# Optimization experiments

Hardware: AMD Instinct MI355X
Metric: run time of the kernel (lower is better)

The kernel has to match this reference:

```python
import jax, jax.numpy as jnp
import numpy as np

A_DIM = 12      # action dim (half of augmented state)
N_STEPS = 10    # Heun ODE steps (Flow.N)
P = 0.95        # mixing coefficient in _Heun_method


def _mlp(x, obs, t, W1, b1, W2, b2, W3, b3, W4, b4):
    h = jnp.concatenate([x, obs, t], axis=-1)
    h = jnp.tanh(h @ W1 + b1)
    h = jnp.tanh(h @ W2 + b2)
    h = jnp.tanh(h @ W3 + b3)
    return h @ W4 + b4


def _heun(obs, x, params):
    # Flow._Heun_method: sequential Heun integration of the augmented state.
    z = x[..., :A_DIM]
    y = x[..., A_DIM:]
    dt = 1.0 / N_STEPS
    tshape = x.shape[:-1] + (1,)

    def step(carry, i):
        z, y = carry
        t = jnp.ones(tshape, x.dtype) * (i / N_STEPS)
        z_t = _mlp(y, obs, t, *params)
        z_in = z + z_t * dt
        y_t = _mlp(z_in, obs, t, *params)
        y_in = y + y_t * dt
        z_new = P * z_in + (1.0 - P) * y_in
        y_new = P * y_in + (1.0 - P) * z_new
        return (z_new, y_new), None

    (z, y), _ = jax.lax.scan(step, (z, y), jnp.arange(N_STEPS, dtype=x.dtype))
    return jnp.concatenate([z, y], axis=-1)


def setup_inputs() -> dict:
    key = jax.random.key(0)
    ks = jax.random.split(key, 8)
    B, OBS, H, A = 2048, 48, 256, A_DIM
    din = A + OBS + 1  # 61
    s = 0.05  # small init scale to keep tanh unsaturated
    return {
        "observations": jax.random.normal(ks[0], (B, OBS), jnp.float32),
        "action_aug_0": jax.random.normal(ks[1], (B, 2 * A), jnp.float32),
        "W1": s * jax.random.normal(ks[2], (din, H), jnp.float32),
        "b1": jnp.zeros((H,), jnp.float32),
        "W2": s * jax.random.normal(ks[3], (H, H), jnp.float32),
        "b2": jnp.zeros((H,), jnp.float32),
        "W3": s * jax.random.normal(ks[4], (H, H), jnp.float32),
        "b3": jnp.zeros((H,), jnp.float32),
        "W4": s * jax.random.normal(ks[5], (H, A), jnp.float32),
        "b4": jnp.zeros((A,), jnp.float32),
        "jac": 1,
    }


def reference(observations, action_aug_0, W1, b1, W2, b2, W3, b3, W4, b4, jac):
    params = (W1, b1, W2, b2, W3, b3, W4, b4)
    action_aug = _heun(observations, action_aug_0, params)
    d = action_aug_0.shape[-1]
    # Normal(0, I) log prob summed over dims
    log_probs = -0.5 * jnp.sum(action_aug_0 ** 2, axis=-1) - 0.5 * d * jnp.log(2.0 * jnp.pi)
    if jac:
        single = lambda o, x: _heun(o, x, params)  # per-sample (obs_dim,), (2a,)
        J = jax.vmap(jax.jacrev(single, argnums=1))(observations, action_aug_0)  # (B, 2a, 2a)
        _, logabsdet = jnp.linalg.slogdet(J)  # = log|det J|
        log_probs = log_probs - logabsdet
    return action_aug, log_probs
```

## Files before the change

kernel.cpp:

```cpp
#include <hip/hip_runtime.h>
#include <hip/hip_bf16.h>


typedef unsigned short ushort_t;
typedef float f32x4 __attribute__((ext_vector_type(4)));
typedef short s16x8 __attribute__((ext_vector_type(8)));

#define NB      2048
#define OBS_D   48
#define XDIM    24
#define NSTEPS  10
#define DT      0.1f
#define PP      0.95f

#define W1U 0
#define W2U 16384
#define W3U 81920
#define W4U 147456
#define FRAG_BLOCKS 592
#define LP_BLOCKS 8

#define LDS_BUFA 0
#define LDS_BUFB 8192
#define LDS_AIN  16384
#define LDS_PART 18432
#define LDS_TOTAL 27648

__device__ __forceinline__ ushort_t f2bf(float f) {
  unsigned u = __builtin_bit_cast(unsigned, f);
  u += 0x7fffu + ((u >> 16) & 1u);
  return (ushort_t)(u >> 16);
}

__device__ __forceinline__ float tanh_fast(float x) {
  float e = __builtin_amdgcn_exp2f(x * 2.885390081777927f);
  return 1.f - 2.f * __builtin_amdgcn_rcpf(1.f + e);
}

__device__ __forceinline__ int ain_byte(int r, int c) {
  int cb = ((c >> 5) << 6) | ((c & 15) << 2) | (((c >> 4) & 1) << 1);
  return r * 128 + (cb ^ ((r & 7) << 4));
}

__global__ void prep_kernel(const float* __restrict__ W1, const float* __restrict__ b1,
                            const float* __restrict__ W2, const float* __restrict__ W3,
                            const float* __restrict__ W4, const float* __restrict__ x0,
                            const int* __restrict__ jac, float* __restrict__ out,
                            ushort_t* __restrict__ ws) {
  int bid = blockIdx.x;
  int tid = threadIdx.x;
  if (bid < FRAG_BLOCKS) {
    int e = bid * 256 + tid;
    float val = 0.f;
    if (e < 16384) {
      int kt = e >> 13; int r = e & 8191;
      int nt = r >> 9, l = (r >> 3) & 63, j = r & 7;
      int k = kt * 32 + ((l >> 4) << 2) + (j >> 1) + ((j & 1) << 4);
      int col = nt * 16 + (l & 15);
      val = (k < 61) ? W1[k * 256 + col] : ((k == 61) ? b1[col] : 0.f);
    } else if (e < 81920) {
      int e2 = e - 16384;
      int kt = e2 >> 13; int r = e2 & 8191;
      int nt = r >> 9, l = (r >> 3) & 63, j = r & 7;
      int k = kt * 32 + ((l >> 4) << 2) + (j >> 1) + ((j & 1) << 4);
      int col = nt * 16 + (l & 15);
      val = W2[k * 256 + col];
    } else if (e < 147456) {
      int e2 = e - 81920;
      int kt = e2 >> 13; int r = e2 & 8191;
      int nt = r >> 9, l = (r >> 3) & 63, j = r & 7;
      int k = kt * 32 + ((l >> 4) << 2) + (j >> 1) + ((j & 1) << 4);
      int col = nt * 16 + (l & 15);
      val = W3[k * 256 + col];
    } else {
      int e2 = e - 147456;
      int kt = e2 >> 9; int r = e2 & 511;
      int l = (r >> 3) & 63, j = r & 7;
      int k = kt * 32 + ((l >> 4) << 2) + (j >> 1) + ((j & 1) << 4);
      int col = l & 15;
      val = (col < 12) ? W4[k * 12 + col] : 0.f;
    }
    ws[e] = f2bf(val);
  } else {
    int s = (bid - FRAG_BLOCKS) * 256 + tid;
    float acc = 0.f;
    #pragma unroll 4
    for (int j = 0; j < XDIM; ++j) { float v = x0[s * XDIM + j]; acc += v * v; }
    float C = (jac[0] != 0) ? -9.744134143900015f : -22.054524796912143f;
    out[NB * XDIM + s] = -0.5f * acc + C;
  }
}

__global__ __launch_bounds__(512, 2) void flow_main(
    const float* __restrict__ obs, const float* __restrict__ x0,
    const float* __restrict__ b2g, const float* __restrict__ b3g,
    const float* __restrict__ b4g, const ushort_t* __restrict__ ws,
    float* __restrict__ out) {
  __shared__ char lds[LDS_TOTAL];
  const int tid  = threadIdx.x;
  const int lane = tid & 63;
  const int wv   = tid >> 6;
  const int g    = lane >> 4;
  const int ar   = lane & 15;
  const int row0 = blockIdx.x * 8;
  const int sw   = (ar & 7) << 4;
  const int hwc  = wv * 64 + ar * 4;
  const int rs   = tid >> 4, cs = tid & 15;

  ((unsigned*)(lds + LDS_AIN))[tid] = 0u;
  __syncthreads();

  if (tid < 8 * OBS_D) {
    int r = tid / OBS_D, o = tid - r * OBS_D;
    *(ushort_t*)(lds + LDS_AIN + ain_byte(r, 12 + o)) = f2bf(obs[(row0 + r) * OBS_D + o]);
  }
  if (tid < 16)
    *(ushort_t*)(lds + LDS_AIN + tid * 128 + (118 ^ ((tid & 7) << 4))) = (ushort_t)0x3F80;

  float zr = 0.f, yr = 0.f, zir = 0.f;
  if (tid < 256 && cs < 12 && rs < 8) {
    zr = x0[(row0 + rs) * XDIM + cs];
    yr = x0[(row0 + rs) * XDIM + 12 + cs];
    *(ushort_t*)(lds + LDS_AIN + rs * 128 + ((cs * 4) ^ ((rs & 7) << 4))) = f2bf(yr);
  }

  s16x8 w1r[2][2], w2r[8][2], w3r[8][2], w4r;
  #pragma unroll
  for (int kt = 0; kt < 2; ++kt)
    #pragma unroll
    for (int n = 0; n < 2; ++n)
      w1r[kt][n] = *(const s16x8*)(ws + W1U + (((kt * 16) + (2 * wv + n)) * 64 + lane) * 8);
  #pragma unroll
  for (int kt = 0; kt < 8; ++kt)
    #pragma unroll
    for (int n = 0; n < 2; ++n) {
      w2r[kt][n] = *(const s16x8*)(ws + W2U + (((kt * 16) + (2 * wv + n)) * 64 + lane) * 8);
      w3r[kt][n] = *(const s16x8*)(ws + W3U + (((kt * 16) + (2 * wv + n)) * 64 + lane) * 8);
    }
  w4r = *(const s16x8*)(ws + W4U + (wv * 64 + lane) * 8);
  #pragma unroll
  for (int kt = 0; kt < 2; ++kt)
    asm volatile("" : "+v"(w1r[kt][0]), "+v"(w1r[kt][1]));
  #pragma unroll
  for (int kt = 0; kt < 8; ++kt)
    asm volatile("" : "+v"(w2r[kt][0]), "+v"(w2r[kt][1]), "+v"(w3r[kt][0]), "+v"(w3r[kt][1]));
  asm volatile("" : "+v"(w4r));

  float b2r[2], b3r[2];
  #pragma unroll
  for (int n = 0; n < 2; ++n) {
    b2r[n] = b2g[(2 * wv + n) * 16 + ar];
    b3r[n] = b3g[(2 * wv + n) * 16 + ar];
  }
  const float b4v = (cs < 12) ? b4g[cs] : 0.f;

  __syncthreads();

  const f32x4 z4 = {0.f, 0.f, 0.f, 0.f};

  for (int i = 0; i < NSTEPS; ++i) {
    #pragma unroll
    for (int ev = 0; ev < 2; ++ev) {
      f32x4 acc0 = z4, acc1 = z4;
      #pragma unroll
      for (int kt = 0; kt < 2; ++kt) {
        s16x8 a = *(const s16x8*)(lds + LDS_AIN + ar * 128 + ((kt * 64 + g * 16) ^ sw));
        acc0 = __builtin_amdgcn_mfma_f32_16x16x32_bf16(a, w1r[kt][0], acc0, 0, 0, 0);
        acc1 = __builtin_amdgcn_mfma_f32_16x16x32_bf16(a, w1r[kt][1], acc1, 0, 0, 0);
      }
      #pragma unroll
      for (int r = 0; r < 4; ++r) {
        int rw = g * 4 + r;
        unsigned p = (unsigned)f2bf(tanh_fast(acc0[r]))
                   | ((unsigned)f2bf(tanh_fast(acc1[r])) << 16);
        *(unsigned*)(lds + LDS_BUFA + rw * 512 + (hwc ^ ((rw & 7) << 4))) = p;
      }
      __syncthreads();

      f32x4 a0a = z4, a0b = z4, a1a = z4, a1b = z4;
      #pragma unroll
      for (int kt = 0; kt < 4; ++kt) {
        s16x8 a = *(const s16x8*)(lds + LDS_BUFA + ar * 512 + ((kt * 64 + g * 16) ^ sw));
        s16x8 b = *(const s16x8*)(lds + LDS_BUFA + ar * 512 + (((kt + 4) * 64 + g * 16) ^ sw));
        a0a = __builtin_amdgcn_mfma_f32_16x16x32_bf16(a, w2r[kt][0], a0a, 0, 0, 0);
        a1a = __builtin_amdgcn_mfma_f32_16x16x32_bf16(a, w2r[kt][1], a1a, 0, 0, 0);
        a0b = __builtin_amdgcn_mfma_f32_16x16x32_bf16(b, w2r[kt + 4][0], a0b, 0, 0, 0);
        a1b = __builtin_amdgcn_mfma_f32_16x16x32_bf16(b, w2r[kt + 4][1], a1b, 0, 0, 0);
      }
      acc0 = a0a + a0b; acc1 = a1a + a1b;
      #pragma unroll
      for (int r = 0; r < 4; ++r) {
        int rw = g * 4 + r;
        unsigned p = (unsigned)f2bf(tanh_fast(acc0[r] + b2r[0]))
                   | ((unsigned)f2bf(tanh_fast(acc1[r] + b2r[1])) << 16);
        *(unsigned*)(lds + LDS_BUFB + rw * 512 + (hwc ^ ((rw & 7) << 4))) = p;
      }
      __syncthreads();

      a0a = z4; a0b = z4; a1a = z4; a1b = z4;
      #pragma unroll
      for (int kt = 0; kt < 4; ++kt) {
        s16x8 a = *(const s16x8*)(lds + LDS_BUFB + ar * 512 + ((kt * 64 + g * 16) ^ sw));
        s16x8 b = *(const s16x8*)(lds + LDS_BUFB + ar * 512 + (((kt + 4) * 64 + g * 16) ^ sw));
        a0a = __builtin_amdgcn_mfma_f32_16x16x32_bf16(a, w3r[kt][0], a0a, 0, 0, 0);
        a1a = __builtin_amdgcn_mfma_f32_16x16x32_bf16(a, w3r[kt][1], a1a, 0, 0, 0);
        a0b = __builtin_amdgcn_mfma_f32_16x16x32_bf16(b, w3r[kt + 4][0], a0b, 0, 0, 0);
        a1b = __builtin_amdgcn_mfma_f32_16x16x32_bf16(b, w3r[kt + 4][1], a1b, 0, 0, 0);
      }
      acc0 = a0a + a0b; acc1 = a1a + a1b;
      #pragma unroll
      for (int r = 0; r < 4; ++r) {
        int rw = g * 4 + r;
        unsigned p = (unsigned)f2bf(tanh_fast(acc0[r] + b3r[0]))
                   | ((unsigned)f2bf(tanh_fast(acc1[r] + b3r[1])) << 16);
        *(unsigned*)(lds + LDS_BUFA + rw * 512 + (hwc ^ ((rw & 7) << 4))) = p;
      }

      asm volatile("s_waitcnt lgkmcnt(0)" ::: "memory");
      __builtin_amdgcn_sched_barrier(0);
      {
        s16x8 a = *(const s16x8*)(lds + LDS_BUFA + ar * 512 + ((wv * 64 + g * 16) ^ sw));
        f32x4 p4 = __builtin_amdgcn_mfma_f32_16x16x32_bf16(a, w4r, z4, 0, 0, 0);
        #pragma unroll
        for (int r = 0; r < 4; ++r) {
          int rw = g * 4 + r;
          *(float*)(lds + LDS_PART + wv * 1152 + rw * 72 + ar * 4) = p4[r];
        }
      }
      __syncthreads();

      if (tid < 256) {
        float s = b4v;
        #pragma unroll
        for (int w = 0; w < 8; ++w)
          s += *(const float*)(lds + LDS_PART + w * 1152 + rs * 72 + cs * 4);
        if (cs < 12) {
          int byt = rs * 128 + ((cs * 4) ^ ((rs & 7) << 4));
          if (ev == 0) {
            zir = zr + DT * s;
            *(ushort_t*)(lds + LDS_AIN + byt) = f2bf(zir);
          } else {
            float yi = yr + DT * s;
            zr = PP * zir + (1.f - PP) * yi;
            yr = PP * yi + (1.f - PP) * zr;
            *(ushort_t*)(lds + LDS_AIN + byt) = f2bf(yr);
          }
        }
        if (ev == 1 && cs == 15)
          *(ushort_t*)(lds + LDS_AIN + rs * 128 + (114 ^ ((rs & 7) << 4))) =
              f2bf((float)(i + 1) * DT);
      }
      __syncthreads();
    }
  }

  if (tid < 256 && cs < 12 && rs < 8) {
    out[(row0 + rs) * XDIM + cs]      = zr;
    out[(row0 + rs) * XDIM + 12 + cs] = yr;
  }
}

extern "C" void kernel_launch(void* const* d_in, const int* in_sizes, int n_in,
                              void* d_out, int out_size, void* d_ws, size_t ws_size,
                              hipStream_t stream) {
  const float* obs = (const float*)d_in[0];
  const float* x0  = (const float*)d_in[1];
  const float* W1  = (const float*)d_in[2];
  const float* b1  = (const float*)d_in[3];
  const float* W2  = (const float*)d_in[4];
  const float* b2  = (const float*)d_in[5];
  const float* W3  = (const float*)d_in[6];
  const float* b3  = (const float*)d_in[7];
  const float* W4  = (const float*)d_in[8];
  const float* b4  = (const float*)d_in[9];
  const int*   jac = (const int*)d_in[10];
  float* out = (float*)d_out;
  ushort_t* ws = (ushort_t*)d_ws;

  prep_kernel<<<FRAG_BLOCKS + LP_BLOCKS, 256, 0, stream>>>(W1, b1, W2, W3, W4, x0, jac, out, ws);
  flow_main<<<256, 512, 0, stream>>>(obs, x0, b2, b3, b4, ws, out);
}
```

Measured before the change: 50.84 us.

## Hoist constant obs/bias layer-1 term, fold tanh scale into weights, process 16 rows per block

Layer 1 is split so the observation and bias contribution is computed once before the time loop, and only a 12-wide action MFMA plus an fp32 time term is applied per evaluation. The tanh exponent scale is folded into the W1/W2/W3 weights and biases, and biases are preloaded into the accumulators. Each block now handles 16 rows instead of 8, so the grid is halved from 256 to 128 blocks. Other changes use packed bf16 conversion and a transposed partial-sum layout that allows vector reads in the reduction. Fewer blocks mean less parallelism on a large GPU, and the time input now stays in fp32 where it was previously rounded to bf16.

```diff
diff --git a/kernel.cpp b/kernel.cpp
--- a/kernel.cpp
+++ b/kernel.cpp
@@ -12,19 +12,21 @@
 #define NSTEPS  10
 #define DT      0.1f
 #define PP      0.95f
-
-#define W1U 0
-#define W2U 16384
-#define W3U 81920
-#define W4U 147456
-#define FRAG_BLOCKS 592
+#define SCL     2.885390081777927f
+
+#define W1U  0
+#define W2U  16384
+#define W3U  81920
+#define W4U  147456
+#define W1AU 151552
+#define FRAG_BLOCKS 624
 #define LP_BLOCKS 8
 
 #define LDS_BUFA 0
 #define LDS_BUFB 8192
 #define LDS_AIN  16384
-#define LDS_PART 18432
-#define LDS_TOTAL 27648
+#define LDS_PART 17408
+#define LDS_TOTAL 25600
 
 __device__ __forceinline__ ushort_t f2bf(float f) {
   unsigned u = __builtin_bit_cast(unsigned, f);
@@ -32,14 +34,13 @@
   return (ushort_t)(u >> 16);
 }
 
-__device__ __forceinline__ float tanh_fast(float x) {
-  float e = __builtin_amdgcn_exp2f(x * 2.885390081777927f);
-  return 1.f - 2.f * __builtin_amdgcn_rcpf(1.f + e);
-}
-
-__device__ __forceinline__ int ain_byte(int r, int c) {
-  int cb = ((c >> 5) << 6) | ((c & 15) << 2) | (((c >> 4) & 1) << 1);
-  return r * 128 + (cb ^ ((r & 7) << 4));
+__device__ __forceinline__ float tanh_s(float u) {
+  float e = __builtin_amdgcn_exp2f(u);
+  return __builtin_fmaf(-2.f, __builtin_amdgcn_rcpf(1.f + e), 1.f);
+}
+
+__device__ __forceinline__ int pair_byte(int c) {
+  return (((c >> 5) << 6) | ((c & 15) << 2) | (((c >> 4) & 1) << 1));
 }
 
 __global__ void prep_kernel(const float* __restrict__ W1, const float* __restrict__ b1,
@@ -57,28 +58,32 @@
       int nt = r >> 9, l = (r >> 3) & 63, j = r & 7;
       int k = kt * 32 + ((l >> 4) << 2) + (j >> 1) + ((j & 1) << 4);
       int col = nt * 16 + (l & 15);
-      val = (k < 61) ? W1[k * 256 + col] : ((k == 61) ? b1[col] : 0.f);
+      val = SCL * ((k < 61) ? W1[k * 256 + col] : ((k == 61) ? b1[col] : 0.f));
     } else if (e < 81920) {
       int e2 = e - 16384;
       int kt = e2 >> 13; int r = e2 & 8191;
       int nt = r >> 9, l = (r >> 3) & 63, j = r & 7;
       int k = kt * 32 + ((l >> 4) << 2) + (j >> 1) + ((j & 1) << 4);
-      int col = nt * 16 + (l & 15);
-      val = W2[k * 256 + col];
+      val = SCL * W2[k * 256 + nt * 16 + (l & 15)];
     } else if (e < 147456) {
       int e2 = e - 81920;
       int kt = e2 >> 13; int r = e2 & 8191;
       int nt = r >> 9, l = (r >> 3) & 63, j = r & 7;
       int k = kt * 32 + ((l >> 4) << 2) + (j >> 1) + ((j & 1) << 4);
-      int col = nt * 16 + (l & 15);
-      val = W3[k * 256 + col];
-    } else {
+      val = SCL * W3[k * 256 + nt * 16 + (l & 15)];
+    } else if (e < 151552) {
       int e2 = e - 147456;
       int kt = e2 >> 9; int r = e2 & 511;
       int l = (r >> 3) & 63, j = r & 7;
       int k = kt * 32 + ((l >> 4) << 2) + (j >> 1) + ((j & 1) << 4);
       int col = l & 15;
       val = (col < 12) ? W4[k * 12 + col] : 0.f;
+    } else {
+      int e2 = e - 151552;
+      int nt = e2 >> 9; int r = e2 & 511;
+      int l = (r >> 3) & 63, j = r & 7;
+      int k = ((l >> 4) << 2) + (j >> 1) + ((j & 1) << 4);
+      val = (k < 12) ? SCL * W1[k * 256 + nt * 16 + (l & 15)] : 0.f;
     }
     ws[e] = f2bf(val);
   } else {
@@ -93,43 +98,48 @@
 
 __global__ __launch_bounds__(512, 2) void flow_main(
     const float* __restrict__ obs, const float* __restrict__ x0,
-    const float* __restrict__ b2g, const float* __restrict__ b3g,
-    const float* __restrict__ b4g, const ushort_t* __restrict__ ws,
-    float* __restrict__ out) {
+    const float* __restrict__ W1g, const float* __restrict__ b2g,
+    const float* __restrict__ b3g, const float* __restrict__ b4g,
+    const ushort_t* __restrict__ ws, float* __restrict__ out) {
   __shared__ char lds[LDS_TOTAL];
   const int tid  = threadIdx.x;
   const int lane = tid & 63;
   const int wv   = tid >> 6;
   const int g    = lane >> 4;
   const int ar   = lane & 15;
-  const int row0 = blockIdx.x * 8;
+  const int row0 = blockIdx.x * 16;
   const int sw   = (ar & 7) << 4;
-  const int hwc  = wv * 64 + ar * 4;
   const int rs   = tid >> 4, cs = tid & 15;
 
-  ((unsigned*)(lds + LDS_AIN))[tid] = 0u;
+  ((unsigned*)(lds + LDS_BUFB))[tid] = 0u;
+  if (tid < 256) ((unsigned*)(lds + LDS_AIN))[tid] = 0u;
   __syncthreads();
 
-  if (tid < 8 * OBS_D) {
-    int r = tid / OBS_D, o = tid - r * OBS_D;
-    *(ushort_t*)(lds + LDS_AIN + ain_byte(r, 12 + o)) = f2bf(obs[(row0 + r) * OBS_D + o]);
+  for (int idx = tid; idx < 16 * OBS_D; idx += 512) {
+    int r = idx / OBS_D, o = idx - r * OBS_D;
+    int byt = pair_byte(12 + o) ^ ((r & 7) << 4);
+    *(ushort_t*)(lds + LDS_BUFB + r * 128 + byt) = f2bf(obs[(row0 + r) * OBS_D + o]);
   }
   if (tid < 16)
-    *(ushort_t*)(lds + LDS_AIN + tid * 128 + (118 ^ ((tid & 7) << 4))) = (ushort_t)0x3F80;
+    *(ushort_t*)(lds + LDS_BUFB + tid * 128 + (pair_byte(61) ^ ((tid & 7) << 4))) = (ushort_t)0x3F80;
 
   float zr = 0.f, yr = 0.f, zir = 0.f;
-  if (tid < 256 && cs < 12 && rs < 8) {
+  if (tid < 256 && cs < 12) {
     zr = x0[(row0 + rs) * XDIM + cs];
     yr = x0[(row0 + rs) * XDIM + 12 + cs];
-    *(ushort_t*)(lds + LDS_AIN + rs * 128 + ((cs * 4) ^ ((rs & 7) << 4))) = f2bf(yr);
-  }
-
-  s16x8 w1r[2][2], w2r[8][2], w3r[8][2], w4r;
+    *(ushort_t*)(lds + LDS_AIN + rs * 64 + ((cs * 4) ^ ((rs & 3) << 4))) = f2bf(yr);
+  }
+
+  s16x8 w1o[2][2];
+  s16x8 w1a[2], w2r[8][2], w3r[8][2], w4r;
   #pragma unroll
   for (int kt = 0; kt < 2; ++kt)
     #pragma unroll
     for (int n = 0; n < 2; ++n)
-      w1r[kt][n] = *(const s16x8*)(ws + W1U + (((kt * 16) + (2 * wv + n)) * 64 + lane) * 8);
+      w1o[kt][n] = *(const s16x8*)(ws + W1U + (((kt * 16) + (2 * wv + n)) * 64 + lane) * 8);
+  #pragma unroll
+  for (int n = 0; n < 2; ++n)
+    w1a[n] = *(const s16x8*)(ws + W1AU + (((2 * wv + n)) * 64 + lane) * 8);
   #pragma unroll
   for (int kt = 0; kt < 8; ++kt)
     #pragma unroll
@@ -138,46 +148,53 @@
       w3r[kt][n] = *(const s16x8*)(ws + W3U + (((kt * 16) + (2 * wv + n)) * 64 + lane) * 8);
     }
   w4r = *(const s16x8*)(ws + W4U + (wv * 64 + lane) * 8);
-  #pragma unroll
-  for (int kt = 0; kt < 2; ++kt)
-    asm volatile("" : "+v"(w1r[kt][0]), "+v"(w1r[kt][1]));
+  asm volatile("" : "+v"(w1a[0]), "+v"(w1a[1]), "+v"(w4r));
   #pragma unroll
   for (int kt = 0; kt < 8; ++kt)
     asm volatile("" : "+v"(w2r[kt][0]), "+v"(w2r[kt][1]), "+v"(w3r[kt][0]), "+v"(w3r[kt][1]));
-  asm volatile("" : "+v"(w4r));
-
-  float b2r[2], b3r[2];
-  #pragma unroll
-  for (int n = 0; n < 2; ++n) {
-    b2r[n] = b2g[(2 * wv + n) * 16 + ar];
-    b3r[n] = b3g[(2 * wv + n) * 16 + ar];
-  }
-  const float b4v = (cs < 12) ? b4g[cs] : 0.f;
+
+  const float w1t0 = SCL * W1g[60 * 256 + 32 * wv + ar];
+  const float w1t1 = SCL * W1g[60 * 256 + 32 * wv + 16 + ar];
+  const float b2s0 = SCL * b2g[32 * wv + ar],      b2s1 = SCL * b2g[32 * wv + 16 + ar];
+  const float b3s0 = SCL * b3g[32 * wv + ar],      b3s1 = SCL * b3g[32 * wv + 16 + ar];
+  const float b4v  = (cs < 12) ? b4g[cs] : 0.f;
 
   __syncthreads();
 
   const f32x4 z4 = {0.f, 0.f, 0.f, 0.f};
+  f32x4 ci0 = z4, ci1 = z4;
+  #pragma unroll
+  for (int kt = 0; kt < 2; ++kt) {
+    s16x8 a = *(const s16x8*)(lds + LDS_BUFB + ar * 128 + ((kt * 64 + g * 16) ^ sw));
+    ci0 = __builtin_amdgcn_mfma_f32_16x16x32_bf16(a, w1o[kt][0], ci0, 0, 0, 0);
+    ci1 = __builtin_amdgcn_mfma_f32_16x16x32_bf16(a, w1o[kt][1], ci1, 0, 0, 0);
+  }
 
   for (int i = 0; i < NSTEPS; ++i) {
+    const float t = (float)i * DT;
+    const float t0 = __builtin_fmaf(t, w1t0, 0.f), t1 = __builtin_fmaf(t, w1t1, 0.f);
     #pragma unroll
     for (int ev = 0; ev < 2; ++ev) {
-      f32x4 acc0 = z4, acc1 = z4;
-      #pragma unroll
-      for (int kt = 0; kt < 2; ++kt) {
-        s16x8 a = *(const s16x8*)(lds + LDS_AIN + ar * 128 + ((kt * 64 + g * 16) ^ sw));
-        acc0 = __builtin_amdgcn_mfma_f32_16x16x32_bf16(a, w1r[kt][0], acc0, 0, 0, 0);
-        acc1 = __builtin_amdgcn_mfma_f32_16x16x32_bf16(a, w1r[kt][1], acc1, 0, 0, 0);
+      f32x4 acc0 = ci0, acc1 = ci1;
+      #pragma unroll
+      for (int r = 0; r < 4; ++r) { acc0[r] += t0; acc1[r] += t1; }
+      {
+        s16x8 a = *(const s16x8*)(lds + LDS_AIN + ar * 64 + ((g * 16) ^ ((ar & 3) << 4)));
+        acc0 = __builtin_amdgcn_mfma_f32_16x16x32_bf16(a, w1a[0], acc0, 0, 0, 0);
+        acc1 = __builtin_amdgcn_mfma_f32_16x16x32_bf16(a, w1a[1], acc1, 0, 0, 0);
       }
       #pragma unroll
       for (int r = 0; r < 4; ++r) {
         int rw = g * 4 + r;
-        unsigned p = (unsigned)f2bf(tanh_fast(acc0[r]))
-                   | ((unsigned)f2bf(tanh_fast(acc1[r])) << 16);
-        *(unsigned*)(lds + LDS_BUFA + rw * 512 + (hwc ^ ((rw & 7) << 4))) = p;
-      }
-      __syncthreads();
-
-      f32x4 a0a = z4, a0b = z4, a1a = z4, a1b = z4;
+        float lo = tanh_s(acc0[r]), hi = tanh_s(acc1[r]);
+        unsigned p;
+        asm("v_cvt_pk_bf16_f32 %0, %1, %2" : "=v"(p) : "v"(lo), "v"(hi));
+        *(unsigned*)(lds + LDS_BUFA + rw * 512 + ((wv * 64 + ar * 4) ^ ((rw & 7) << 4))) = p;
+      }
+      __syncthreads();
+
+      f32x4 a0a = {b2s0, b2s0, b2s0, b2s0}, a1a = {b2s1, b2s1, b2s1, b2s1};
+      f32x4 a0b = z4, a1b = z4;
       #pragma unroll
       for (int kt = 0; kt < 4; ++kt) {
         s16x8 a = *(const s16x8*)(lds + LDS_BUFA + ar * 512 + ((kt * 64 + g * 16) ^ sw));
@@ -191,13 +208,15 @@
       #pragma unroll
       for (int r = 0; r < 4; ++r) {
         int rw = g * 4 + r;
-        unsigned p = (unsigned)f2bf(tanh_fast(acc0[r] + b2r[0]))
-                   | ((unsigned)f2bf(tanh_fast(acc1[r] + b2r[1])) << 16);
-        *(unsigned*)(lds + LDS_BUFB + rw * 512 + (hwc ^ ((rw & 7) << 4))) = p;
-      }
-      __syncthreads();
-
-      a0a = z4; a0b = z4; a1a = z4; a1b = z4;
+        float lo = tanh_s(acc0[r]), hi = tanh_s(acc1[r]);
+        unsigned p;
+        asm("v_cvt_pk_bf16_f32 %0, %1, %2" : "=v"(p) : "v"(lo), "v"(hi));
+        *(unsigned*)(lds + LDS_BUFB + rw * 512 + ((wv * 64 + ar * 4) ^ ((rw & 7) << 4))) = p;
+      }
+      __syncthreads();
+
+      a0a = (f32x4){b3s0, b3s0, b3s0, b3s0}; a1a = (f32x4){b3s1, b3s1, b3s1, b3s1};
+      a0b = z4; a1b = z4;
       #pragma unroll
       for (int kt = 0; kt < 4; ++kt) {
         s16x8 a = *(const s16x8*)(lds + LDS_BUFB + ar * 512 + ((kt * 64 + g * 16) ^ sw));
@@ -211,9 +230,10 @@
       #pragma unroll
       for (int r = 0; r < 4; ++r) {
         int rw = g * 4 + r;
-        unsigned p = (unsigned)f2bf(tanh_fast(acc0[r] + b3r[0]))
-                   | ((unsigned)f2bf(tanh_fast(acc1[r] + b3r[1])) << 16);
-        *(unsigned*)(lds + LDS_BUFA + rw * 512 + (hwc ^ ((rw & 7) << 4))) = p;
+        float lo = tanh_s(acc0[r]), hi = tanh_s(acc1[r]);
+        unsigned p;
+        asm("v_cvt_pk_bf16_f32 %0, %1, %2" : "=v"(p) : "v"(lo), "v"(hi));
+        *(unsigned*)(lds + LDS_BUFA + rw * 512 + ((wv * 64 + ar * 4) ^ ((rw & 7) << 4))) = p;
       }
 
       asm volatile("s_waitcnt lgkmcnt(0)" ::: "memory");
@@ -222,20 +242,19 @@
         s16x8 a = *(const s16x8*)(lds + LDS_BUFA + ar * 512 + ((wv * 64 + g * 16) ^ sw));
         f32x4 p4 = __builtin_amdgcn_mfma_f32_16x16x32_bf16(a, w4r, z4, 0, 0, 0);
         #pragma unroll
-        for (int r = 0; r < 4; ++r) {
-          int rw = g * 4 + r;
-          *(float*)(lds + LDS_PART + wv * 1152 + rw * 72 + ar * 4) = p4[r];
-        }
+        for (int r = 0; r < 4; ++r)
+          *(float*)(lds + LDS_PART + (((g * 4 + r) * 128 + ar * 8 + wv) << 2)) = p4[r];
       }
       __syncthreads();
 
       if (tid < 256) {
-        float s = b4v;
-        #pragma unroll
-        for (int w = 0; w < 8; ++w)
-          s += *(const float*)(lds + LDS_PART + w * 1152 + rs * 72 + cs * 4);
+        const char* pb = lds + LDS_PART + ((rs * 128 + cs * 8) << 2);
+        f32x4 va = *(const f32x4*)pb;
+        f32x4 vb = *(const f32x4*)(pb + 16);
+        f32x4 sv = va + vb;
+        float s = ((sv[0] + sv[1]) + (sv[2] + sv[3])) + b4v;
         if (cs < 12) {
-          int byt = rs * 128 + ((cs * 4) ^ ((rs & 7) << 4));
+          int byt = rs * 64 + ((cs * 4) ^ ((rs & 3) << 4));
           if (ev == 0) {
             zir = zr + DT * s;
             *(ushort_t*)(lds + LDS_AIN + byt) = f2bf(zir);
@@ -246,15 +265,12 @@
             *(ushort_t*)(lds + LDS_AIN + byt) = f2bf(yr);
           }
         }
-        if (ev == 1 && cs == 15)
-          *(ushort_t*)(lds + LDS_AIN + rs * 128 + (114 ^ ((rs & 7) << 4))) =
-              f2bf((float)(i + 1) * DT);
       }
       __syncthreads();
     }
   }
 
-  if (tid < 256 && cs < 12 && rs < 8) {
+  if (tid < 256 && cs < 12) {
     out[(row0 + rs) * XDIM + cs]      = zr;
     out[(row0 + rs) * XDIM + 12 + cs] = yr;
   }
@@ -278,5 +294,5 @@
   ushort_t* ws = (ushort_t*)d_ws;
 
   prep_kernel<<<FRAG_BLOCKS + LP_BLOCKS, 256, 0, stream>>>(W1, b1, W2, W3, W4, x0, jac, out, ws);
-  flow_main<<<256, 512, 0, stream>>>(obs, x0, b2, b3, b4, ws, out);
-}
+  flow_main<<<128, 512, 0, stream>>>(obs, x0, W1, b2, b3, b4, ws, out);
+}
```

Measured after the change: 48.55 us. -4.5%, faster.
